# Optimization experiments

Hardware: AMD Instinct MI355X
Metric: run time of the kernel (lower is better)

## Reference

```python
import jax, jax.numpy as jnp
import numpy as np

N = 50000   # num_nodes
E = 800000  # num_edges (avg degree 16)
D = 128     # input_dim
H = 128     # hidden_dim
EPS = 1e-5


def _linear_params(key, fan_in, fan_out):
    k1, k2 = jax.random.split(key)
    s = 1.0 / np.sqrt(fan_in)
    W = jax.random.uniform(k1, (fan_in, fan_out), jnp.float32, -s, s)
    b = jax.random.uniform(k2, (fan_out,), jnp.float32, -s, s)
    return W, b


def setup_inputs() -> dict:
    key = jax.random.key(0)
    ks = jax.random.split(key, 10)
    x = jax.random.normal(ks[0], (N, D), jnp.float32)
    edge_index = jax.random.randint(ks[1], (2, E), 0, N)
    edge_weight = jax.random.uniform(ks[2], (E,), jnp.float32)
    W1, b1 = _linear_params(ks[3], D, H)
    W2, b2 = _linear_params(ks[4], H, H)
    W3, b3 = _linear_params(ks[5], H, H)
    Wh, bh = _linear_params(ks[6], H, H)
    Wa, ba = _linear_params(ks[7], H, 1)
    Wz, bz = _linear_params(ks[8], H, 1)
    ones = jnp.ones((H,), jnp.float32)
    zeros = jnp.zeros((H,), jnp.float32)
    return dict(x=x, edge_index=edge_index, edge_weight=edge_weight,
                W1=W1, b1=b1, W2=W2, b2=b2, W3=W3, b3=b3,
                g1=ones, be1=zeros, g2=ones, be2=zeros, g3=ones, be3=zeros,
                Wh=Wh, bh=bh, Wa=Wa, ba=ba, Wz=Wz, bz=bz)


def _batchnorm(h, g, b):
    mu = jnp.mean(h, axis=0)
    var = jnp.mean((h - mu) ** 2, axis=0)  # biased, as torch BN training
    return (h - mu) * jax.lax.rsqrt(var + EPS) * g + b


def reference(x, edge_index, edge_weight,
              W1, b1, W2, b2, W3, b3,
              g1, be1, g2, be2, g3, be3,
              Wh, bh, Wa, ba, Wz, bz):
    row, col = edge_index[0], edge_index[1]
    loop = jnp.arange(N)
    row_f = jnp.concatenate([row, loop])   # sources (with self-loops)
    col_f = jnp.concatenate([col, loop])   # targets
    w_f = jnp.concatenate([edge_weight, jnp.ones((N,), edge_weight.dtype)])
    deg = jax.ops.segment_sum(w_f, col_f, num_segments=N)
    dinv = jnp.where(deg > 0, jax.lax.rsqrt(deg), 0.0)
    norm = dinv[row_f] * w_f * dinv[col_f]  # [E+N]

    def conv(h, W, b):
        hw = h @ W  # [N,H]
        msg = hw[row_f] * norm[:, None]  # gather + scale
        return jax.ops.segment_sum(msg, col_f, num_segments=N) + b  # scatter-add

    h = jax.nn.relu(_batchnorm(conv(x, W1, b1), g1, be1))
    h = jax.nn.relu(_batchnorm(conv(h, W2, b2), g2, be2))
    h = jax.nn.relu(_batchnorm(conv(h, W3, b3), g3, be3))
    # dropout is identity in eval
    h = jax.nn.relu(h @ Wh + bh)
    ace = h[0] @ Wa + ba  # target_indices[0]
    h2 = h[1] @ Wz + bz   # target_indices[1]
    return jnp.concatenate([ace, h2], axis=0)  # [2]
```

## Files before the change

kernel.cpp:

```cpp
#include <hip/hip_runtime.h>


typedef unsigned short u16;
typedef unsigned int u32;
typedef unsigned long long u64;
typedef short bf16x8 __attribute__((ext_vector_type(8)));
typedef float f32x4 __attribute__((ext_vector_type(4)));

#define NREP 64

__device__ inline float bf2f(u16 u) { return __uint_as_float(((u32)u) << 16); }
__device__ inline u16 f2bf(float f) {
  u32 u = __float_as_uint(f);
  return (u16)((u + 0x7FFFu + ((u >> 16) & 1u)) >> 16);
}

__global__ __launch_bounds__(256) void k_zero_cnt(int* cnt, int n) {
  int i = blockIdx.x * 256 + threadIdx.x;
  if (i < n) cnt[i] = 0;
}

__global__ __launch_bounds__(256) void k_count_rank(const int* __restrict__ col,
                                                    int* __restrict__ cnt,
                                                    int* __restrict__ rank, int e) {
  int i = blockIdx.x * 256 + threadIdx.x;
  if (i < e) rank[i] = atomicAdd(&cnt[col[i]], 1);
}

__global__ __launch_bounds__(256) void k_scan1(const int* __restrict__ cnt,
                                               int* __restrict__ ptr,
                                               int* __restrict__ bsum, int n) {
  __shared__ int sh[256];
  int t = threadIdx.x;
  int i = blockIdx.x * 256 + t;
  int v = (i < n) ? cnt[i] : 0;
  sh[t] = v;
  __syncthreads();
  for (int d = 1; d < 256; d <<= 1) {
    int u = (t >= d) ? sh[t - d] : 0;
    __syncthreads();
    sh[t] += u;
    __syncthreads();
  }
  if (i < n) ptr[i] = sh[t] - v;
  if (t == 255) bsum[blockIdx.x] = sh[255];
}

__global__ __launch_bounds__(256) void k_scan2(int* __restrict__ bsum, int nb) {
  __shared__ int sh[256];
  int t = threadIdx.x;
  int v = (t < nb) ? bsum[t] : 0;
  sh[t] = v;
  __syncthreads();
  for (int d = 1; d < 256; d <<= 1) {
    int u = (t >= d) ? sh[t - d] : 0;
    __syncthreads();
    sh[t] += u;
    __syncthreads();
  }
  if (t < nb) bsum[t] = sh[t] - v;
}

__global__ __launch_bounds__(256) void k_scan3(int* __restrict__ ptr,
                                               const int* __restrict__ bsum,
                                               int n, int e) {
  int i = blockIdx.x * 256 + threadIdx.x;
  if (i < n) ptr[i] += bsum[blockIdx.x];
  if (i == 0) ptr[n] = e;
}

__global__ __launch_bounds__(256) void k_fill(const int* __restrict__ row,
                                              const int* __restrict__ col,
                                              const float* __restrict__ w,
                                              const int* __restrict__ ptr,
                                              const int* __restrict__ rank,
                                              int2* __restrict__ emeta, int e) {
  int i = blockIdx.x * 256 + threadIdx.x;
  if (i < e) {
    int pos = ptr[col[i]] + rank[i];
    emeta[pos] = make_int2(row[i], __float_as_int(w[i]));
  }
}

__global__ __launch_bounds__(256) void k_deg_dinv(const int* __restrict__ ptr,
                                                  const int2* __restrict__ emeta,
                                                  float* __restrict__ dinv, int n) {
  int i = blockIdx.x * 256 + threadIdx.x;
  if (i >= n) return;
  int j = ptr[i], end = ptr[i + 1];
  float d = 1.0f;
  for (; j < end; ++j) d += __int_as_float(emeta[j].y);
  dinv[i] = rsqrtf(d);
}

__global__ __launch_bounds__(256) void k_coef(const int* __restrict__ ptr,
                                              int2* __restrict__ emeta,
                                              const float* __restrict__ dinv, int n) {
  int i = blockIdx.x * 256 + threadIdx.x;
  if (i >= n) return;
  float dc = dinv[i];
  int j = ptr[i], end = ptr[i + 1];
  for (; j < end; ++j) {
    int2 m = emeta[j];
    emeta[j] = make_int2(m.x, __float_as_int(dinv[m.x] * __int_as_float(m.y) * dc));
  }
}

__global__ __launch_bounds__(256) void k_gemm(const void* __restrict__ Ain,
                                              int a_is_f32,
                                              const float* __restrict__ W,
                                              u16* __restrict__ C,
                                              const float* __restrict__ ab,
                                              float* __restrict__ Szero,
                                              int n) {
  __shared__ u64 As64[128 * 32];
  __shared__ u64 Ws64[128 * 32];
  __shared__ float absh[256];
  int t = threadIdx.x;
  if (blockIdx.x < 16) {
#pragma unroll
    for (int i = 0; i < 4; ++i)
      Szero[blockIdx.x * 1024 + t + 256 * i] = 0.f;
  }
  if (ab) {
    if (t < 128) {
      absh[t] = ab[t];
      absh[128 + t] = ab[128 + t];
    }
    __syncthreads();
  }

  int row0 = blockIdx.x * 128;
  int nr = min(128, n - row0);

  if (a_is_f32) {
    const float4* src = (const float4*)((const float*)Ain + (size_t)row0 * 128);
#pragma unroll
    for (int i = 0; i < 16; ++i) {
      int idx = t + 256 * i;
      int r = idx >> 5;
      int j4 = idx & 31;
      float4 v = (r < nr) ? src[idx] : make_float4(0.f, 0.f, 0.f, 0.f);
      u64 cell = (u64)f2bf(v.x) | ((u64)f2bf(v.y) << 16) |
                 ((u64)f2bf(v.z) << 32) | ((u64)f2bf(v.w) << 48);
      As64[r * 32 + (j4 ^ (r & 15))] = cell;
    }
  } else {
    const u16* A = (const u16*)Ain;
#pragma unroll
    for (int i = 0; i < 8; ++i) {
      int idx = t + 256 * i;
      int r = idx >> 4;
      int c8 = idx & 15;
      u64 lo = 0, hi = 0;
      if (r < nr) {
        const u64* srcq = (const u64*)(A + ((size_t)(row0 + r)) * 128 + c8 * 8);
        lo = srcq[0]; hi = srcq[1];
        if (ab) {
          u64 nl = 0, nh = 0;
#pragma unroll
          for (int j = 0; j < 4; ++j) {
            int c = c8 * 8 + j;
            float f = fmaxf(fmaf(bf2f((u16)(lo >> (16 * j))), absh[c], absh[128 + c]), 0.f);
            nl |= ((u64)f2bf(f)) << (16 * j);
            int c2 = c + 4;
            float f2 = fmaxf(fmaf(bf2f((u16)(hi >> (16 * j))), absh[c2], absh[128 + c2]), 0.f);
            nh |= ((u64)f2bf(f2)) << (16 * j);
          }
          lo = nl; hi = nh;
        }
      }
      As64[r * 32 + ((c8 * 2) ^ (r & 15))] = lo;
      As64[r * 32 + ((c8 * 2 + 1) ^ (r & 15))] = hi;
    }
  }
  {
    int col = t & 127;
    int khalf = t >> 7;
#pragma unroll
    for (int kk = 0; kk < 16; ++kk) {
      int k4 = khalf * 16 + kk;
      int k = k4 * 4;
      u64 cell = (u64)f2bf(W[(size_t)(k + 0) * 128 + col]) |
                 ((u64)f2bf(W[(size_t)(k + 1) * 128 + col]) << 16) |
                 ((u64)f2bf(W[(size_t)(k + 2) * 128 + col]) << 32) |
                 ((u64)f2bf(W[(size_t)(k + 3) * 128 + col]) << 48);
      Ws64[col * 32 + (k4 ^ (col & 15))] = cell;
    }
  }
  __syncthreads();

  int w = t >> 6, l = t & 63;
  int lr = l & 15, kg = l >> 4;
  int rA0 = w * 32 + lr, rA1 = rA0 + 16;
  f32x4 acc[2][8];
#pragma unroll
  for (int m = 0; m < 2; ++m)
#pragma unroll
    for (int nf = 0; nf < 8; ++nf) acc[m][nf] = (f32x4){0.f, 0.f, 0.f, 0.f};

  union Frag { u64 q[2]; bf16x8 v; };
#pragma unroll
  for (int ks = 0; ks < 4; ++ks) {
    int kb = ks * 8 + kg;
    Frag a0, a1;
    a0.q[0] = As64[rA0 * 32 + (kb ^ lr)];
    a0.q[1] = As64[rA0 * 32 + ((kb + 4) ^ lr)];
    a1.q[0] = As64[rA1 * 32 + (kb ^ lr)];
    a1.q[1] = As64[rA1 * 32 + ((kb + 4) ^ lr)];
#pragma unroll
    for (int nf = 0; nf < 8; ++nf) {
      Frag b;
      b.q[0] = Ws64[(nf * 16 + lr) * 32 + (kb ^ lr)];
      b.q[1] = Ws64[(nf * 16 + lr) * 32 + ((kb + 4) ^ lr)];
      acc[0][nf] = __builtin_amdgcn_mfma_f32_16x16x32_bf16(a0.v, b.v, acc[0][nf], 0, 0, 0);
      acc[1][nf] = __builtin_amdgcn_mfma_f32_16x16x32_bf16(a1.v, b.v, acc[1][nf], 0, 0, 0);
    }
  }
#pragma unroll
  for (int m = 0; m < 2; ++m)
#pragma unroll
    for (int nf = 0; nf < 8; ++nf)
#pragma unroll
      for (int j = 0; j < 4; ++j) {
        int gr = row0 + w * 32 + m * 16 + kg * 4 + j;
        if (gr < n) C[(size_t)gr * 128 + nf * 16 + lr] = f2bf(acc[m][nf][j]);
      }
}

__global__ __launch_bounds__(256) void k_gather(const u16* __restrict__ hw,
                                                const int* __restrict__ ptr,
                                                const int2* __restrict__ emeta,
                                                const float* __restrict__ dinv,
                                                u16* __restrict__ out,
                                                float* __restrict__ stats, int n) {
  int w = threadIdx.x >> 6;
  int lane = threadIdx.x & 63;
  float sx = 0.f, sy = 0.f, sxx = 0.f, syy = 0.f;
#pragma unroll
  for (int it = 0; it < 4; ++it) {
    int node = blockIdx.x * 16 + it * 4 + w;
    if (node < n) {
      float di = dinv[node];
      u32 su = ((const u32*)(hw + (size_t)node * 128))[lane];
      float ax = bf2f((u16)su) * di * di;
      float ay = bf2f((u16)(su >> 16)) * di * di;
      int j = ptr[node], end = ptr[node + 1];
      for (; j + 3 < end; j += 4) {
        int2 m0 = emeta[j], m1 = emeta[j + 1], m2 = emeta[j + 2], m3 = emeta[j + 3];
        float c0 = __int_as_float(m0.y), c1 = __int_as_float(m1.y);
        float c2 = __int_as_float(m2.y), c3 = __int_as_float(m3.y);
        u32 v0 = ((const u32*)(hw + (size_t)m0.x * 128))[lane];
        u32 v1 = ((const u32*)(hw + (size_t)m1.x * 128))[lane];
        u32 v2 = ((const u32*)(hw + (size_t)m2.x * 128))[lane];
        u32 v3 = ((const u32*)(hw + (size_t)m3.x * 128))[lane];
        ax = fmaf(bf2f((u16)v0), c0, ax); ay = fmaf(bf2f((u16)(v0 >> 16)), c0, ay);
        ax = fmaf(bf2f((u16)v1), c1, ax); ay = fmaf(bf2f((u16)(v1 >> 16)), c1, ay);
        ax = fmaf(bf2f((u16)v2), c2, ax); ay = fmaf(bf2f((u16)(v2 >> 16)), c2, ay);
        ax = fmaf(bf2f((u16)v3), c3, ax); ay = fmaf(bf2f((u16)(v3 >> 16)), c3, ay);
      }
      for (; j < end; ++j) {
        int2 m0 = emeta[j];
        float c0 = __int_as_float(m0.y);
        u32 v0 = ((const u32*)(hw + (size_t)m0.x * 128))[lane];
        ax = fmaf(bf2f((u16)v0), c0, ax); ay = fmaf(bf2f((u16)(v0 >> 16)), c0, ay);
      }
      u32 o = (u32)f2bf(ax) | ((u32)f2bf(ay) << 16);
      ((u32*)(out + (size_t)node * 128))[lane] = o;
      sx += ax; sy += ay;
      sxx = fmaf(ax, ax, sxx); syy = fmaf(ay, ay, syy);
    }
  }
  __shared__ float4 red[256];
  red[threadIdx.x] = make_float4(sx, sy, sxx, syy);
  __syncthreads();
  if (threadIdx.x < 64) {
    int t = threadIdx.x;
    float4 a = red[t], b = red[t + 64], c = red[t + 128], d = red[t + 192];
    float* S = stats + (blockIdx.x & (NREP - 1)) * 256;
    unsafeAtomicAdd(&S[2 * t],           a.x + b.x + c.x + d.x);
    unsafeAtomicAdd(&S[2 * t + 1],       a.y + b.y + c.y + d.y);
    unsafeAtomicAdd(&S[128 + 2 * t],     a.z + b.z + c.z + d.z);
    unsafeAtomicAdd(&S[128 + 2 * t + 1], a.w + b.w + c.w + d.w);
  }
}

__global__ __launch_bounds__(128) void k_bn_finalize(const float* __restrict__ S,
                                                     const float* __restrict__ g,
                                                     const float* __restrict__ be,
                                                     float* __restrict__ ab, int n) {
  int c = threadIdx.x;
  float s = 0.f, ss = 0.f;
#pragma unroll 8
  for (int r = 0; r < NREP; ++r) {
    s += S[r * 256 + c];
    ss += S[r * 256 + 128 + c];
  }
  float inv_n = 1.0f / (float)n;
  float mu = s * inv_n;
  float var = ss * inv_n - mu * mu;
  float istd = rsqrtf(var + 1e-5f);
  float A = g[c] * istd;
  ab[c] = A;
  ab[128 + c] = fmaf(-mu, A, be[c]);
}

__global__ __launch_bounds__(256) void k_head(const u16* __restrict__ h,
                                              const float* __restrict__ ab,
                                              const float* __restrict__ Wh,
                                              const float* __restrict__ bh,
                                              const float* __restrict__ Wa,
                                              const float* __restrict__ ba,
                                              const float* __restrict__ Wz,
                                              const float* __restrict__ bz,
                                              float* __restrict__ out) {
  __shared__ float hrow[256];
  __shared__ float red[256];
  int t = threadIdx.x;
  {
    int c = t & 127;
    hrow[t] = fmaxf(fmaf(bf2f(h[t]), ab[c], ab[128 + c]), 0.f);
  }
  __syncthreads();
  int j = t & 127, r = t >> 7;
  float acc = bh[j];
  for (int k = 0; k < 128; ++k)
    acc = fmaf(hrow[r * 128 + k], Wh[k * 128 + j], acc);
  float hv = fmaxf(acc, 0.f);
  float wv = (r == 0) ? Wa[j] : Wz[j];
  red[t] = hv * wv;
  __syncthreads();
  for (int s = 64; s >= 1; s >>= 1) {
    if (j < s) red[t] += red[t + s];
    __syncthreads();
  }
  if (t == 0) out[0] = red[0] + ba[0];
  if (t == 128) out[1] = red[128] + bz[0];
}

extern "C" void kernel_launch(void* const* d_in, const int* in_sizes, int n_in,
                              void* d_out, int out_size, void* d_ws, size_t ws_size,
                              hipStream_t stream) {
  const float* x  = (const float*)d_in[0];
  const int*   ei = (const int*)d_in[1];
  const float* ew = (const float*)d_in[2];
  const float* W[3]  = {(const float*)d_in[3], (const float*)d_in[5], (const float*)d_in[7]};
  const float* g[3]  = {(const float*)d_in[9],  (const float*)d_in[11], (const float*)d_in[13]};
  const float* be[3] = {(const float*)d_in[10], (const float*)d_in[12], (const float*)d_in[14]};
  const float* Wh = (const float*)d_in[15];
  const float* bh = (const float*)d_in[16];
  const float* Wa = (const float*)d_in[17];
  const float* ba = (const float*)d_in[18];
  const float* Wz = (const float*)d_in[19];
  const float* bz = (const float*)d_in[20];

  const int n = in_sizes[0] / 128;
  const int e = in_sizes[1] / 2;
  const int* row = ei;
  const int* col = ei + e;

  u16*   hw_b   = (u16*)d_ws;
  u16*   hbuf_b = hw_b + (size_t)n * 128;
  float* dinv   = (float*)(hbuf_b + (size_t)n * 128);
  float* stats3 = dinv + n;
  float* ab     = stats3 + 3 * NREP * 256;
  int*   cnt    = (int*)(ab + 3 * 256);
  int*   ptr    = cnt + n;
  int*   bsum   = ptr + n + 1;
  int*   rank   = bsum + 256;
  uintptr_t pm  = ((uintptr_t)(rank + e) + 15) & ~(uintptr_t)15;
  int2*  emeta  = (int2*)pm;

  const int nb_n = (n + 255) / 256;
  const int nb_e = (e + 255) / 256;

  k_zero_cnt<<<nb_n, 256, 0, stream>>>(cnt, n);
  k_count_rank<<<nb_e, 256, 0, stream>>>(col, cnt, rank, e);
  k_scan1<<<nb_n, 256, 0, stream>>>(cnt, ptr, bsum, n);
  k_scan2<<<1, 256, 0, stream>>>(bsum, nb_n);
  k_scan3<<<nb_n, 256, 0, stream>>>(ptr, bsum, n, e);
  k_fill<<<nb_e, 256, 0, stream>>>(row, col, ew, ptr, rank, emeta, e);
  k_deg_dinv<<<nb_n, 256, 0, stream>>>(ptr, emeta, dinv, n);
  k_coef<<<nb_n, 256, 0, stream>>>(ptr, emeta, dinv, n);

  for (int l = 0; l < 3; ++l) {
    const void* hin = (l == 0) ? (const void*)x : (const void*)hbuf_b;
    const float* abp = (l == 0) ? nullptr : (ab + (l - 1) * 256);
    k_gemm<<<(n + 127) / 128, 256, 0, stream>>>(hin, (l == 0) ? 1 : 0, W[l],
                                                hw_b, abp,
                                                stats3 + l * NREP * 256, n);
    k_gather<<<(n + 15) / 16, 256, 0, stream>>>(hw_b, ptr, emeta, dinv, hbuf_b,
                                                stats3 + l * NREP * 256, n);
    k_bn_finalize<<<1, 128, 0, stream>>>(stats3 + l * NREP * 256, g[l], be[l],
                                         ab + l * 256, n);
  }
  k_head<<<1, 256, 0, stream>>>(hbuf_b, ab + 2 * 256, Wh, bh, Wa, ba, Wz, bz,
                                (float*)d_out);
}
```

Measured before the change: 377.3 us.

## Prepack bf16 weight tiles once and pre-shift gather row offsets

A new kernel converts the three weight matrices to bf16 in the swizzled LDS cell layout once per call. Each GEMM block now copies those cells straight into shared memory instead of doing strided fp32 loads and conversions. Source indices in the edge metadata are stored pre-shifted by 8 so the gather computes byte addresses with a single add. The gather also splits each accumulator into two chains for more ILP and uses cheaper bf16-to-float bit ops. The costs are one extra small launch and a shifted row index that caps node counts at about 2^23.

```diff
diff --git a/kernel.cpp b/kernel.cpp
--- a/kernel.cpp
+++ b/kernel.cpp
@@ -78,7 +78,7 @@
   int i = blockIdx.x * 256 + threadIdx.x;
   if (i < e) {
     int pos = ptr[col[i]] + rank[i];
-    emeta[pos] = make_int2(row[i], __float_as_int(w[i]));
+    emeta[pos] = make_int2(row[i] << 8, __float_as_int(w[i]));
   }
 }
 
@@ -102,13 +102,35 @@
   int j = ptr[i], end = ptr[i + 1];
   for (; j < end; ++j) {
     int2 m = emeta[j];
-    emeta[j] = make_int2(m.x, __float_as_int(dinv[m.x] * __int_as_float(m.y) * dc));
+    emeta[j] = make_int2(m.x,
+        __float_as_int(dinv[m.x >> 8] * __int_as_float(m.y) * dc));
+  }
+}
+
+__global__ __launch_bounds__(256) void k_wpack(const float* __restrict__ W0,
+                                               const float* __restrict__ W1,
+                                               const float* __restrict__ W2,
+                                               u64* __restrict__ cells) {
+  const float* W = (blockIdx.x == 0) ? W0 : (blockIdx.x == 1) ? W1 : W2;
+  u64* out = cells + (size_t)blockIdx.x * 4096;
+  int t = threadIdx.x;
+#pragma unroll
+  for (int i = 0; i < 16; ++i) {
+    int cell = t + 256 * i;
+    int col = cell >> 5;
+    int k4 = cell & 31;
+    int k = k4 * 4;
+    u64 c = (u64)f2bf(W[(size_t)(k + 0) * 128 + col]) |
+            ((u64)f2bf(W[(size_t)(k + 1) * 128 + col]) << 16) |
+            ((u64)f2bf(W[(size_t)(k + 2) * 128 + col]) << 32) |
+            ((u64)f2bf(W[(size_t)(k + 3) * 128 + col]) << 48);
+    out[col * 32 + (k4 ^ (col & 15))] = c;
   }
 }
 
 __global__ __launch_bounds__(256) void k_gemm(const void* __restrict__ Ain,
                                               int a_is_f32,
-                                              const float* __restrict__ W,
+                                              const u64* __restrict__ Wc,
                                               u16* __restrict__ C,
                                               const float* __restrict__ ab,
                                               float* __restrict__ Szero,
@@ -122,12 +144,17 @@
     for (int i = 0; i < 4; ++i)
       Szero[blockIdx.x * 1024 + t + 256 * i] = 0.f;
   }
+  {
+    const ulonglong2* src = (const ulonglong2*)Wc;
+    ulonglong2* dst = (ulonglong2*)Ws64;
+#pragma unroll
+    for (int i = 0; i < 8; ++i) dst[t + 256 * i] = src[t + 256 * i];
+  }
   if (ab) {
     if (t < 128) {
       absh[t] = ab[t];
       absh[128 + t] = ab[128 + t];
     }
-    __syncthreads();
   }
 
   int row0 = blockIdx.x * 128;
@@ -147,6 +174,7 @@
     }
   } else {
     const u16* A = (const u16*)Ain;
+    __syncthreads();
 #pragma unroll
     for (int i = 0; i < 8; ++i) {
       int idx = t + 256 * i;
@@ -174,20 +202,6 @@
       As64[r * 32 + ((c8 * 2 + 1) ^ (r & 15))] = hi;
     }
   }
-  {
-    int col = t & 127;
-    int khalf = t >> 7;
-#pragma unroll
-    for (int kk = 0; kk < 16; ++kk) {
-      int k4 = khalf * 16 + kk;
-      int k = k4 * 4;
-      u64 cell = (u64)f2bf(W[(size_t)(k + 0) * 128 + col]) |
-                 ((u64)f2bf(W[(size_t)(k + 1) * 128 + col]) << 16) |
-                 ((u64)f2bf(W[(size_t)(k + 2) * 128 + col]) << 32) |
-                 ((u64)f2bf(W[(size_t)(k + 3) * 128 + col]) << 48);
-      Ws64[col * 32 + (k4 ^ (col & 15))] = cell;
-    }
-  }
   __syncthreads();
 
   int w = t >> 6, l = t & 63;
@@ -235,38 +249,46 @@
                                                 u16* __restrict__ out,
                                                 float* __restrict__ stats, int n) {
   int w = threadIdx.x >> 6;
-  int lane = threadIdx.x & 63;
+  int lane4 = (threadIdx.x & 63) * 4;
+  const char* hwb = (const char*)hw;
   float sx = 0.f, sy = 0.f, sxx = 0.f, syy = 0.f;
 #pragma unroll
   for (int it = 0; it < 4; ++it) {
     int node = blockIdx.x * 16 + it * 4 + w;
     if (node < n) {
       float di = dinv[node];
-      u32 su = ((const u32*)(hw + (size_t)node * 128))[lane];
-      float ax = bf2f((u16)su) * di * di;
-      float ay = bf2f((u16)(su >> 16)) * di * di;
+      u32 su = *(const u32*)(hwb + ((size_t)node << 8) + lane4);
+      float ax0 = __uint_as_float(su << 16) * di * di;
+      float ay0 = __uint_as_float(su & 0xFFFF0000u) * di * di;
+      float ax1 = 0.f, ay1 = 0.f;
       int j = ptr[node], end = ptr[node + 1];
       for (; j + 3 < end; j += 4) {
         int2 m0 = emeta[j], m1 = emeta[j + 1], m2 = emeta[j + 2], m3 = emeta[j + 3];
         float c0 = __int_as_float(m0.y), c1 = __int_as_float(m1.y);
         float c2 = __int_as_float(m2.y), c3 = __int_as_float(m3.y);
-        u32 v0 = ((const u32*)(hw + (size_t)m0.x * 128))[lane];
-        u32 v1 = ((const u32*)(hw + (size_t)m1.x * 128))[lane];
-        u32 v2 = ((const u32*)(hw + (size_t)m2.x * 128))[lane];
-        u32 v3 = ((const u32*)(hw + (size_t)m3.x * 128))[lane];
-        ax = fmaf(bf2f((u16)v0), c0, ax); ay = fmaf(bf2f((u16)(v0 >> 16)), c0, ay);
-        ax = fmaf(bf2f((u16)v1), c1, ax); ay = fmaf(bf2f((u16)(v1 >> 16)), c1, ay);
-        ax = fmaf(bf2f((u16)v2), c2, ax); ay = fmaf(bf2f((u16)(v2 >> 16)), c2, ay);
-        ax = fmaf(bf2f((u16)v3), c3, ax); ay = fmaf(bf2f((u16)(v3 >> 16)), c3, ay);
+        u32 v0 = *(const u32*)(hwb + m0.x + lane4);
+        u32 v1 = *(const u32*)(hwb + m1.x + lane4);
+        u32 v2 = *(const u32*)(hwb + m2.x + lane4);
+        u32 v3 = *(const u32*)(hwb + m3.x + lane4);
+        ax0 = fmaf(__uint_as_float(v0 << 16), c0, ax0);
+        ay0 = fmaf(__uint_as_float(v0 & 0xFFFF0000u), c0, ay0);
+        ax1 = fmaf(__uint_as_float(v1 << 16), c1, ax1);
+        ay1 = fmaf(__uint_as_float(v1 & 0xFFFF0000u), c1, ay1);
+        ax0 = fmaf(__uint_as_float(v2 << 16), c2, ax0);
+        ay0 = fmaf(__uint_as_float(v2 & 0xFFFF0000u), c2, ay0);
+        ax1 = fmaf(__uint_as_float(v3 << 16), c3, ax1);
+        ay1 = fmaf(__uint_as_float(v3 & 0xFFFF0000u), c3, ay1);
       }
       for (; j < end; ++j) {
         int2 m0 = emeta[j];
         float c0 = __int_as_float(m0.y);
-        u32 v0 = ((const u32*)(hw + (size_t)m0.x * 128))[lane];
-        ax = fmaf(bf2f((u16)v0), c0, ax); ay = fmaf(bf2f((u16)(v0 >> 16)), c0, ay);
+        u32 v0 = *(const u32*)(hwb + m0.x + lane4);
+        ax0 = fmaf(__uint_as_float(v0 << 16), c0, ax0);
+        ay0 = fmaf(__uint_as_float(v0 & 0xFFFF0000u), c0, ay0);
       }
+      float ax = ax0 + ax1, ay = ay0 + ay1;
       u32 o = (u32)f2bf(ax) | ((u32)f2bf(ay) << 16);
-      ((u32*)(out + (size_t)node * 128))[lane] = o;
+      *(u32*)((char*)out + ((size_t)node << 8) + lane4) = o;
       sx += ax; sy += ay;
       sxx = fmaf(ax, ax, sxx); syy = fmaf(ay, ay, syy);
     }
@@ -364,7 +386,8 @@
   float* dinv   = (float*)(hbuf_b + (size_t)n * 128);
   float* stats3 = dinv + n;
   float* ab     = stats3 + 3 * NREP * 256;
-  int*   cnt    = (int*)(ab + 3 * 256);
+  u64*   wcells = (u64*)(ab + 3 * 256);
+  int*   cnt    = (int*)(wcells + 3 * 4096);
   int*   ptr    = cnt + n;
   int*   bsum   = ptr + n + 1;
   int*   rank   = bsum + 256;
@@ -382,11 +405,13 @@
   k_fill<<<nb_e, 256, 0, stream>>>(row, col, ew, ptr, rank, emeta, e);
   k_deg_dinv<<<nb_n, 256, 0, stream>>>(ptr, emeta, dinv, n);
   k_coef<<<nb_n, 256, 0, stream>>>(ptr, emeta, dinv, n);
+  k_wpack<<<3, 256, 0, stream>>>(W[0], W[1], W[2], wcells);
 
   for (int l = 0; l < 3; ++l) {
     const void* hin = (l == 0) ? (const void*)x : (const void*)hbuf_b;
     const float* abp = (l == 0) ? nullptr : (ab + (l - 1) * 256);
-    k_gemm<<<(n + 127) / 128, 256, 0, stream>>>(hin, (l == 0) ? 1 : 0, W[l],
+    k_gemm<<<(n + 127) / 128, 256, 0, stream>>>(hin, (l == 0) ? 1 : 0,
+                                                wcells + (size_t)l * 4096,
                                                 hw_b, abp,
                                                 stats3 + l * NREP * 256, n);
     k_gather<<<(n + 15) / 16, 256, 0, stream>>>(hw_b, ptr, emeta, dinv, hbuf_b,
```

Measured after the change: 385.5 us. 2.2% more time.
